# Performance work log

Measured on AMD Instinct MI355X. Metric: run time of the kernel, lower is better.

Reference implementation:

```python
import jax, jax.numpy as jnp
import numpy as np

EPS = 1e-8
LAM = 0.7  # resonance_lambda


def phase_resonance(a, b, eps=EPS):
    # a, b: (B, N, D) float32. Pairwise phase coherence -> (B, N, N)
    D = a.shape[-1]
    pairs = (D // 2)
    a2 = a[..., :pairs * 2].reshape(*a.shape[:-1], pairs, 2)
    b2 = b[..., :pairs * 2].reshape(*b.shape[:-1], pairs, 2)
    theta_a = jnp.arctan2(a2[..., 1] + eps, a2[..., 0] + eps)  # (B,N,pairs)
    theta_b = jnp.arctan2(b2[..., 1] + eps, b2[..., 0] + eps)  # (B,N,pairs)
    delta = theta_a[:, :, None, :] - theta_b[:, None, :, :]    # (B,N,N,pairs)
    return jnp.cos(delta).mean(axis=-1)                        # (B,N,N)


def setup_inputs() -> dict:
    key = jax.random.key(0)
    k1, k2, k3, k4, k5 = jax.random.split(key, 5)
    B, N, D = 2, 1024, 128
    node_states = jax.random.normal(k1, (B, N, D), dtype=jnp.float32)
    node_gates = jax.random.uniform(k2, (B, N, 1), dtype=jnp.float32)
    r_acc = jax.random.normal(k3, (B, N, N), dtype=jnp.float32)
    # nn.Linear(D, D, bias=False) weights, y = x @ W.T
    scale = 1.0 / np.sqrt(D)
    W_in = jax.random.uniform(k4, (D, D), dtype=jnp.float32, minval=-scale, maxval=scale)
    W_out = jax.random.uniform(k5, (D, D), dtype=jnp.float32, minval=-scale, maxval=scale)
    conductance = jnp.asarray(1.0, dtype=jnp.float32)
    return {"node_states": node_states, "node_gates": node_gates, "r_acc": r_acc,
            "W_in": W_in, "W_out": W_out, "conductance": conductance}


def reference(node_states, node_gates, r_acc, W_in, W_out, conductance):
    B, N, D = node_states.shape
    h = node_states @ W_in.T                                   # field_in projection
    r_instant = phase_resonance(h, h)                          # (B,N,N)
    r_acc_new = LAM * r_acc + (1.0 - LAM) * r_instant
    r_acc_new = jnp.clip(r_acc_new, -2.0, 2.0)
    cond = jnp.clip(conductance, -5.0, 5.0)
    coupling = jax.nn.sigmoid(cond * r_acc_new)                # (B,N,N)
    eye = jnp.eye(N, dtype=coupling.dtype)[None]               # zero self-coupling
    coupling = coupling * (1.0 - eye)
    coupling = coupling * jnp.swapaxes(node_gates, -1, -2)     # (B,1,N) col gates
    coupling = coupling * node_gates                           # (B,N,1) row gates
    coupling = coupling / (coupling.sum(axis=-1, keepdims=True) + 1e-8)
    transmitted = node_states * node_gates
    values = transmitted @ W_out.T                             # field_out projection
    field_signal = coupling @ values                           # (B,N,D)
    return field_signal, r_acc_new
```

## Files before the change

kernel.cpp:

```cpp
#include <hip/hip_runtime.h>
#include <hip/hip_bf16.h>

using bf16x8 = __attribute__((ext_vector_type(8))) short;
using f32x4  = __attribute__((ext_vector_type(4))) float;

#define NN 1024
#define DD 128

__device__ __forceinline__ short bf16b(float f) {
    __hip_bfloat16 t = __float2bfloat16(f);
    return *(short*)&t;
}

__device__ __forceinline__ bf16x8 cvt8(const float* __restrict__ p) {
    float4 a = *(const float4*)p;
    float4 b = *(const float4*)(p + 4);
    bf16x8 r;
    r[0] = bf16b(a.x); r[1] = bf16b(a.y); r[2] = bf16b(a.z); r[3] = bf16b(a.w);
    r[4] = bf16b(b.x); r[5] = bf16b(b.y); r[6] = bf16b(b.z); r[7] = bf16b(b.w);
    return r;
}

__global__ __launch_bounds__(256) void prep_kernel(
    const float* __restrict__ states, const float* __restrict__ gates,
    const float* __restrict__ W_in, const float* __restrict__ W_out,
    __hip_bfloat16* __restrict__ M_bf, __hip_bfloat16* __restrict__ valT)
{
    __shared__ __align__(16) short s_m[16][136];
    __shared__ __align__(16) short s_vT[128][24];

    const int tid = threadIdx.x;
    const int l = tid & 63, w = tid >> 6;
    const int row_a = l & 15, kg = l >> 4;
    const int b  = blockIdx.x >> 6;
    const int n0 = (blockIdx.x & 63) * 16;
    const int colbase = w * 32;

    const float* A = states + ((size_t)b * NN + n0) * DD;

    f32x4 accH[2], accV[2];
    #pragma unroll
    for (int cp = 0; cp < 2; ++cp) {
        accH[cp] = (f32x4){0.f, 0.f, 0.f, 0.f};
        accV[cp] = (f32x4){0.f, 0.f, 0.f, 0.f};
    }

    #pragma unroll
    for (int ks = 0; ks < 4; ++ks) {
        int koff = (ks * 4 + kg) * 8;
        bf16x8 a = cvt8(A + row_a * DD + koff);
        #pragma unroll
        for (int cp = 0; cp < 2; ++cp) {
            int d = colbase + cp * 16 + row_a;
            bf16x8 b1 = cvt8(W_in  + d * DD + koff);
            bf16x8 b2 = cvt8(W_out + d * DD + koff);
            accH[cp] = __builtin_amdgcn_mfma_f32_16x16x32_bf16(a, b1, accH[cp], 0, 0, 0);
            accV[cp] = __builtin_amdgcn_mfma_f32_16x16x32_bf16(a, b2, accV[cp], 0, 0, 0);
        }
    }

    float g[4];
    #pragma unroll
    for (int q = 0; q < 4; ++q) g[q] = gates[b * NN + n0 + kg * 4 + q];

    const bool odd = (row_a & 1) != 0;
    #pragma unroll
    for (int cp = 0; cp < 2; ++cp) {
        #pragma unroll
        for (int q = 0; q < 4; ++q) {
            float hm = accH[cp][q] + 1e-8f;
            float hp = __shfl_xor(hm, 1);
            float x = odd ? hp : hm;
            float y = odd ? hm : hp;
            float r2 = x * x + y * y;
            float out;
            if (r2 > 0.f) out = (odd ? y : x) * rsqrtf(r2);
            else          out = odd ? 0.f : 1.f;
            s_m[kg * 4 + q][colbase + cp * 16 + row_a] = bf16b(out);
            s_vT[colbase + cp * 16 + row_a][kg * 4 + q] = bf16b(accV[cp][q] * g[q]);
        }
    }
    __syncthreads();

    {
        int r = tid >> 4, seg = tid & 15;
        bf16x8 v = *(const bf16x8*)&s_m[r][seg * 8];
        *(bf16x8*)(M_bf + ((size_t)b * NN + n0 + r) * DD + seg * 8) = v;
    }
    {
        int d = tid >> 1, half = tid & 1;
        bf16x8 v = *(const bf16x8*)&s_vT[d][half * 8];
        *(bf16x8*)(valT + ((size_t)b * DD + d) * NN + n0 + half * 8) = v;
    }
}

__global__ __launch_bounds__(256) void fused_kernel(
    const __hip_bfloat16* __restrict__ M_bf,
    const __hip_bfloat16* __restrict__ valT,
    const float* __restrict__ r_acc,
    const float* __restrict__ gates,
    const float* __restrict__ cond_ptr,
    float* __restrict__ r_out,
    __hip_bfloat16* __restrict__ part,
    float* __restrict__ part_rs)
{
    __shared__ __align__(16) short s_cpl[16][136];
    __shared__ float s_rs[16][4];

    const int tid = threadIdx.x;
    const int l = tid & 63, w = tid >> 6;
    const int row_a = l & 15, kg = l >> 4;
    const int jq = blockIdx.x;
    const int j0 = jq * 128;
    const int i0 = blockIdx.y * 16;
    const int b  = blockIdx.z;

    const bf16x8* Mv = (const bf16x8*)(M_bf + (size_t)b * NN * DD);
    const bf16x8* Vv = (const bf16x8*)(valT + (size_t)b * DD * NN);

    f32x4 acc[2];
    acc[0] = (f32x4){0.f, 0.f, 0.f, 0.f};
    acc[1] = (f32x4){0.f, 0.f, 0.f, 0.f};
    #pragma unroll
    for (int ks = 0; ks < 4; ++ks) {
        bf16x8 a = Mv[(size_t)(i0 + row_a) * 16 + ks * 4 + kg];
        #pragma unroll
        for (int cp = 0; cp < 2; ++cp) {
            bf16x8 bb = Mv[(size_t)(j0 + w * 32 + cp * 16 + row_a) * 16 + ks * 4 + kg];
            acc[cp] = __builtin_amdgcn_mfma_f32_16x16x32_bf16(a, bb, acc[cp], 0, 0, 0);
        }
    }

    const float cond = fminf(fmaxf(cond_ptr[0], -5.f), 5.f);
    float g_i[4], g_j[2];
    #pragma unroll
    for (int q = 0; q < 4; ++q) g_i[q] = gates[(size_t)b * NN + i0 + kg * 4 + q];
    #pragma unroll
    for (int cp = 0; cp < 2; ++cp) g_j[cp] = gates[(size_t)b * NN + j0 + w * 32 + cp * 16 + row_a];

    const size_t robase = (size_t)b * NN * NN;
    float rs[4] = {0.f, 0.f, 0.f, 0.f};

    #pragma unroll
    for (int q = 0; q < 4; ++q) {
        const int i = i0 + kg * 4 + q;
        const float gi = g_i[q];
        #pragma unroll
        for (int cp = 0; cp < 2; ++cp) {
            const int jl = w * 32 + cp * 16 + row_a;
            const int j  = j0 + jl;
            float s  = acc[cp][q] * (1.f / 64.f);
            float ra = r_acc[robase + (size_t)i * NN + j];
            float rn = fminf(fmaxf(0.7f * ra + 0.3f * s, -2.f), 2.f);
            r_out[robase + (size_t)i * NN + j] = rn;
            float cpl = (i == j) ? 0.f
                        : (1.f / (1.f + __expf(-cond * rn))) * gi * g_j[cp];
            rs[q] += cpl;
            s_cpl[kg * 4 + q][jl] = bf16b(cpl);
        }
    }

    #pragma unroll
    for (int q = 0; q < 4; ++q) {
        float v = rs[q];
        v += __shfl_xor(v, 1);
        v += __shfl_xor(v, 2);
        v += __shfl_xor(v, 4);
        v += __shfl_xor(v, 8);
        if (row_a == 0) s_rs[kg * 4 + q][w] = v;
    }
    __syncthreads();

    f32x4 pacc[2];
    pacc[0] = (f32x4){0.f, 0.f, 0.f, 0.f};
    pacc[1] = (f32x4){0.f, 0.f, 0.f, 0.f};
    #pragma unroll
    for (int ks2 = 0; ks2 < 4; ++ks2) {
        bf16x8 a = *(const bf16x8*)&s_cpl[row_a][(ks2 * 4 + kg) * 8];
        #pragma unroll
        for (int dt = 0; dt < 2; ++dt) {
            int d = w * 32 + dt * 16 + row_a;
            bf16x8 bb = Vv[(size_t)d * (NN / 8) + (j0 >> 3) + ks2 * 4 + kg];
            pacc[dt] = __builtin_amdgcn_mfma_f32_16x16x32_bf16(a, bb, pacc[dt], 0, 0, 0);
        }
    }

    __hip_bfloat16* pb = part + ((size_t)jq * 2 + b) * NN * DD;
    #pragma unroll
    for (int dt = 0; dt < 2; ++dt) {
        #pragma unroll
        for (int q = 0; q < 4; ++q) {
            int i = i0 + kg * 4 + q;
            int d = w * 32 + dt * 16 + row_a;
            pb[(size_t)i * DD + d] = __float2bfloat16(pacc[dt][q]);
        }
    }

    if (tid < 16)
        part_rs[((size_t)jq * 2 + b) * NN + i0 + tid] =
            s_rs[tid][0] + s_rs[tid][1] + s_rs[tid][2] + s_rs[tid][3];
}

__global__ __launch_bounds__(256) void reduce_kernel(
    const __hip_bfloat16* __restrict__ part,
    const float* __restrict__ part_rs,
    float* __restrict__ field)
{
    int t   = blockIdx.x * 256 + threadIdx.x;
    int b   = t >> 15;
    int rem = t & 32767;
    int i   = rem >> 5;
    int d4  = (rem & 31) * 4;
    size_t ibase = (size_t)i * DD + d4;

    float s0 = 0.f, s1 = 0.f, s2 = 0.f, s3 = 0.f, rsum = 0.f;
    #pragma unroll
    for (int jq = 0; jq < 8; ++jq) {
        size_t slab = ((size_t)jq * 2 + b);
        uint2 u = *(const uint2*)(part + slab * NN * DD + ibase);
        s0 += __uint_as_float(u.x << 16);
        s1 += __uint_as_float(u.x & 0xffff0000u);
        s2 += __uint_as_float(u.y << 16);
        s3 += __uint_as_float(u.y & 0xffff0000u);
        rsum += part_rs[slab * NN + i];
    }
    float inv = 1.0f / (rsum + 1e-8f);
    float4 o = {s0 * inv, s1 * inv, s2 * inv, s3 * inv};
    *(float4*)(field + ((size_t)b * NN + i) * DD + d4) = o;
}

extern "C" void kernel_launch(void* const* d_in, const int* in_sizes, int n_in,
                              void* d_out, int out_size, void* d_ws, size_t ws_size,
                              hipStream_t stream) {
    const float* states = (const float*)d_in[0];
    const float* gates  = (const float*)d_in[1];
    const float* r_acc  = (const float*)d_in[2];
    const float* W_in   = (const float*)d_in[3];
    const float* W_out  = (const float*)d_in[4];
    const float* cond   = (const float*)d_in[5];

    float* field = (float*)d_out;
    float* r_out = field + 2 * NN * DD;

    char* ws = (char*)d_ws;
    __hip_bfloat16* M_bf    = (__hip_bfloat16*)ws;
    __hip_bfloat16* valT    = (__hip_bfloat16*)(ws + (512 << 10));
    __hip_bfloat16* part    = (__hip_bfloat16*)(ws + (1 << 20));
    float*          part_rs = (float*)(ws + (5 << 20));

    hipLaunchKernelGGL(prep_kernel, dim3(128), dim3(256), 0, stream,
                       states, gates, W_in, W_out, M_bf, valT);
    hipLaunchKernelGGL(fused_kernel, dim3(8, 64, 2), dim3(256), 0, stream,
                       M_bf, valT, r_acc, gates, cond, r_out, part, part_rs);
    hipLaunchKernelGGL(reduce_kernel, dim3(256), dim3(256), 0, stream,
                       part, part_rs, field);
}
```

Baseline: 97.73 us.

## Split prep into more blocks, prefetch r_acc early, widen reduce grid

The prep kernel now runs 512 one-wave blocks, each handling a 32-column slice, instead of 128 four-wave blocks, so more CUs share the projection work. The fused kernel loads all MFMA operands and the r_acc tile up front, before the matmul, so the global loads overlap the compute, and it sets a min-blocks-per-CU hint of 4. The reduce kernel uses twice as many threads, each handling two elements, to get more parallelism. Narrower loads and stores in reduce and the extra registers used by the prefetch may offset some of the gain.

Measured after the change: 95.30 us (median of 2 runs). 2.5% less time.

```diff
diff --git a/kernel.cpp b/kernel.cpp
--- a/kernel.cpp
+++ b/kernel.cpp
@@ -21,20 +21,19 @@
     return r;
 }
 
-__global__ __launch_bounds__(256) void prep_kernel(
+__global__ __launch_bounds__(64) void prep_kernel(
     const float* __restrict__ states, const float* __restrict__ gates,
     const float* __restrict__ W_in, const float* __restrict__ W_out,
     __hip_bfloat16* __restrict__ M_bf, __hip_bfloat16* __restrict__ valT)
 {
-    __shared__ __align__(16) short s_m[16][136];
-    __shared__ __align__(16) short s_vT[128][24];
+    __shared__ __align__(16) short s_m[16][32];
+    __shared__ __align__(16) short s_vT[32][16];
 
     const int tid = threadIdx.x;
-    const int l = tid & 63, w = tid >> 6;
-    const int row_a = l & 15, kg = l >> 4;
-    const int b  = blockIdx.x >> 6;
-    const int n0 = (blockIdx.x & 63) * 16;
-    const int colbase = w * 32;
+    const int row_a = tid & 15, kg = tid >> 4;
+    const int c0 = blockIdx.x * 32;
+    const int n0 = blockIdx.y * 16;
+    const int b  = blockIdx.z;
 
     const float* A = states + ((size_t)b * NN + n0) * DD;
 
@@ -51,7 +50,7 @@
         bf16x8 a = cvt8(A + row_a * DD + koff);
         #pragma unroll
         for (int cp = 0; cp < 2; ++cp) {
-            int d = colbase + cp * 16 + row_a;
+            int d = c0 + cp * 16 + row_a;
             bf16x8 b1 = cvt8(W_in  + d * DD + koff);
             bf16x8 b2 = cvt8(W_out + d * DD + koff);
             accH[cp] = __builtin_amdgcn_mfma_f32_16x16x32_bf16(a, b1, accH[cp], 0, 0, 0);
@@ -76,25 +75,25 @@
             float out;
             if (r2 > 0.f) out = (odd ? y : x) * rsqrtf(r2);
             else          out = odd ? 0.f : 1.f;
-            s_m[kg * 4 + q][colbase + cp * 16 + row_a] = bf16b(out);
-            s_vT[colbase + cp * 16 + row_a][kg * 4 + q] = bf16b(accV[cp][q] * g[q]);
+            s_m[kg * 4 + q][cp * 16 + row_a] = bf16b(out);
+            s_vT[cp * 16 + row_a][kg * 4 + q] = bf16b(accV[cp][q] * g[q]);
         }
     }
     __syncthreads();
 
     {
-        int r = tid >> 4, seg = tid & 15;
+        int r = tid >> 2, seg = tid & 3;
         bf16x8 v = *(const bf16x8*)&s_m[r][seg * 8];
-        *(bf16x8*)(M_bf + ((size_t)b * NN + n0 + r) * DD + seg * 8) = v;
+        *(bf16x8*)(M_bf + ((size_t)b * NN + n0 + r) * DD + c0 + seg * 8) = v;
     }
     {
         int d = tid >> 1, half = tid & 1;
         bf16x8 v = *(const bf16x8*)&s_vT[d][half * 8];
-        *(bf16x8*)(valT + ((size_t)b * DD + d) * NN + n0 + half * 8) = v;
-    }
-}
-
-__global__ __launch_bounds__(256) void fused_kernel(
+        *(bf16x8*)(valT + ((size_t)b * DD + c0 + d) * NN + n0 + half * 8) = v;
+    }
+}
+
+__global__ __launch_bounds__(256, 4) void fused_kernel(
     const __hip_bfloat16* __restrict__ M_bf,
     const __hip_bfloat16* __restrict__ valT,
     const float* __restrict__ r_acc,
@@ -118,29 +117,43 @@
     const bf16x8* Mv = (const bf16x8*)(M_bf + (size_t)b * NN * DD);
     const bf16x8* Vv = (const bf16x8*)(valT + (size_t)b * DD * NN);
 
+    bf16x8 aF[4], bF[4][2];
+    #pragma unroll
+    for (int ks = 0; ks < 4; ++ks) {
+        aF[ks] = Mv[(size_t)(i0 + row_a) * 16 + ks * 4 + kg];
+        #pragma unroll
+        for (int cp = 0; cp < 2; ++cp)
+            bF[ks][cp] = Mv[(size_t)(j0 + w * 32 + cp * 16 + row_a) * 16 + ks * 4 + kg];
+    }
+
+    const size_t robase = (size_t)b * NN * NN;
+    float ra[4][2];
+    #pragma unroll
+    for (int q = 0; q < 4; ++q) {
+        const int i = i0 + kg * 4 + q;
+        #pragma unroll
+        for (int cp = 0; cp < 2; ++cp)
+            ra[q][cp] = r_acc[robase + (size_t)i * NN + j0 + w * 32 + cp * 16 + row_a];
+    }
+
+    const float cond = fminf(fmaxf(cond_ptr[0], -5.f), 5.f);
+    float g_i[4], g_j[2];
+    #pragma unroll
+    for (int q = 0; q < 4; ++q) g_i[q] = gates[(size_t)b * NN + i0 + kg * 4 + q];
+    #pragma unroll
+    for (int cp = 0; cp < 2; ++cp) g_j[cp] = gates[(size_t)b * NN + j0 + w * 32 + cp * 16 + row_a];
+
     f32x4 acc[2];
     acc[0] = (f32x4){0.f, 0.f, 0.f, 0.f};
     acc[1] = (f32x4){0.f, 0.f, 0.f, 0.f};
     #pragma unroll
     for (int ks = 0; ks < 4; ++ks) {
-        bf16x8 a = Mv[(size_t)(i0 + row_a) * 16 + ks * 4 + kg];
-        #pragma unroll
-        for (int cp = 0; cp < 2; ++cp) {
-            bf16x8 bb = Mv[(size_t)(j0 + w * 32 + cp * 16 + row_a) * 16 + ks * 4 + kg];
-            acc[cp] = __builtin_amdgcn_mfma_f32_16x16x32_bf16(a, bb, acc[cp], 0, 0, 0);
-        }
-    }
-
-    const float cond = fminf(fmaxf(cond_ptr[0], -5.f), 5.f);
-    float g_i[4], g_j[2];
-    #pragma unroll
-    for (int q = 0; q < 4; ++q) g_i[q] = gates[(size_t)b * NN + i0 + kg * 4 + q];
-    #pragma unroll
-    for (int cp = 0; cp < 2; ++cp) g_j[cp] = gates[(size_t)b * NN + j0 + w * 32 + cp * 16 + row_a];
-
-    const size_t robase = (size_t)b * NN * NN;
+        #pragma unroll
+        for (int cp = 0; cp < 2; ++cp)
+            acc[cp] = __builtin_amdgcn_mfma_f32_16x16x32_bf16(aF[ks], bF[ks][cp], acc[cp], 0, 0, 0);
+    }
+
     float rs[4] = {0.f, 0.f, 0.f, 0.f};
-
     #pragma unroll
     for (int q = 0; q < 4; ++q) {
         const int i = i0 + kg * 4 + q;
@@ -150,8 +163,7 @@
             const int jl = w * 32 + cp * 16 + row_a;
             const int j  = j0 + jl;
             float s  = acc[cp][q] * (1.f / 64.f);
-            float ra = r_acc[robase + (size_t)i * NN + j];
-            float rn = fminf(fmaxf(0.7f * ra + 0.3f * s, -2.f), 2.f);
+            float rn = fminf(fmaxf(0.7f * ra[q][cp] + 0.3f * s, -2.f), 2.f);
             r_out[robase + (size_t)i * NN + j] = rn;
             float cpl = (i == j) ? 0.f
                         : (1.f / (1.f + __expf(-cond * rn))) * gi * g_j[cp];
@@ -190,9 +202,9 @@
     for (int dt = 0; dt < 2; ++dt) {
         #pragma unroll
         for (int q = 0; q < 4; ++q) {
-            int i = i0 + kg * 4 + q;
-            int d = w * 32 + dt * 16 + row_a;
-            pb[(size_t)i * DD + d] = __float2bfloat16(pacc[dt][q]);
+            int ii = i0 + kg * 4 + q;
+            int d  = w * 32 + dt * 16 + row_a;
+            pb[(size_t)ii * DD + d] = __float2bfloat16(pacc[dt][q]);
         }
     }
 
@@ -207,26 +219,24 @@
     float* __restrict__ field)
 {
     int t   = blockIdx.x * 256 + threadIdx.x;
-    int b   = t >> 15;
-    int rem = t & 32767;
-    int i   = rem >> 5;
-    int d4  = (rem & 31) * 4;
-    size_t ibase = (size_t)i * DD + d4;
-
-    float s0 = 0.f, s1 = 0.f, s2 = 0.f, s3 = 0.f, rsum = 0.f;
+    int b   = t >> 16;
+    int rem = t & 65535;
+    int i   = rem >> 6;
+    int d2  = (rem & 63) * 2;
+    size_t ibase = (size_t)i * DD + d2;
+
+    float s0 = 0.f, s1 = 0.f, rsum = 0.f;
     #pragma unroll
     for (int jq = 0; jq < 8; ++jq) {
         size_t slab = ((size_t)jq * 2 + b);
-        uint2 u = *(const uint2*)(part + slab * NN * DD + ibase);
-        s0 += __uint_as_float(u.x << 16);
-        s1 += __uint_as_float(u.x & 0xffff0000u);
-        s2 += __uint_as_float(u.y << 16);
-        s3 += __uint_as_float(u.y & 0xffff0000u);
+        unsigned int u = *(const unsigned int*)(part + slab * NN * DD + ibase);
+        s0 += __uint_as_float(u << 16);
+        s1 += __uint_as_float(u & 0xffff0000u);
         rsum += part_rs[slab * NN + i];
     }
     float inv = 1.0f / (rsum + 1e-8f);
-    float4 o = {s0 * inv, s1 * inv, s2 * inv, s3 * inv};
-    *(float4*)(field + ((size_t)b * NN + i) * DD + d4) = o;
+    float2 o = {s0 * inv, s1 * inv};
+    *(float2*)(field + ((size_t)b * NN + i) * DD + d2) = o;
 }
 
 extern "C" void kernel_launch(void* const* d_in, const int* in_sizes, int n_in,
@@ -248,10 +258,10 @@
     __hip_bfloat16* part    = (__hip_bfloat16*)(ws + (1 << 20));
     float*          part_rs = (float*)(ws + (5 << 20));
 
-    hipLaunchKernelGGL(prep_kernel, dim3(128), dim3(256), 0, stream,
+    hipLaunchKernelGGL(prep_kernel, dim3(4, 64, 2), dim3(64), 0, stream,
                        states, gates, W_in, W_out, M_bf, valT);
     hipLaunchKernelGGL(fused_kernel, dim3(8, 64, 2), dim3(256), 0, stream,
                        M_bf, valT, r_acc, gates, cond, r_out, part, part_rs);
-    hipLaunchKernelGGL(reduce_kernel, dim3(256), dim3(256), 0, stream,
+    hipLaunchKernelGGL(reduce_kernel, dim3(512), dim3(256), 0, stream,
                        part, part_rs, field);
 }
```
